# Performance work log

Hardware: AMD Instinct MI355X
Metric: run time of the kernel (lower is better)

The kernel has to match this reference:

```python
import jax, jax.numpy as jnp
import numpy as np

NUM_HEADS = 8
WIN = (7, 7)


def _relative_position_index(wh, ww):
    # Same construction as the torch module (numpy, static).
    coords = np.stack(np.meshgrid(np.arange(wh), np.arange(ww), indexing='ij'))  # (2, wh, ww)
    flat = coords.reshape(2, -1)                                                 # (2, L)
    rel = flat[:, :, None] - flat[:, None, :]                                    # (2, L, L)
    rel = rel.transpose(1, 2, 0).astype(np.int64)                                # (L, L, 2)
    rel[:, :, 0] += wh - 1
    rel[:, :, 1] += ww - 1
    rel[:, :, 0] *= 2 * ww - 1
    return rel.sum(-1)  # (L, L), values in [0, (2wh-1)*(2ww-1))


def setup_inputs() -> dict:
    key = jax.random.key(0)
    k0, k1, k2, k3, k4 = jax.random.split(key, 5)
    B, C = 2048, 256
    wh, ww = WIN
    L = wh * ww
    nW = 64
    q = jax.random.normal(k0, (B, C, wh, ww), dtype=jnp.float32)
    k = jax.random.normal(k1, (B, C, wh, ww), dtype=jnp.float32)
    v = jax.random.normal(k2, (B, C, wh, ww), dtype=jnp.float32)
    # Swin-style shift mask: 0 where attend, -100 where blocked
    keep = jax.random.uniform(k3, (nW, L, L)) < 0.9
    mask = jnp.where(keep, 0.0, -100.0).astype(jnp.float32)
    n_bias = (2 * wh - 1) * (2 * ww - 1)  # 169
    rel_bias_table = 0.02 * jax.random.normal(k4, (n_bias, NUM_HEADS), dtype=jnp.float32)
    rel_pos_index = jnp.asarray(_relative_position_index(wh, ww), dtype=jnp.int32)
    return {"q": q, "k": k, "v": v, "mask": mask,
            "rel_bias_table": rel_bias_table, "rel_pos_index": rel_pos_index}


def reference(q, k, v, mask, rel_bias_table, rel_pos_index):
    b, c, wh, ww = q.shape
    L = wh * ww
    H = NUM_HEADS
    d_k = c // H
    scale = d_k ** -0.5
    qh = q.reshape(b, H, d_k, L)
    kh = k.reshape(b, H, d_k, L)
    # NOTE: the original torch code reassigns v = k.reshape(...) — values come from k.
    vh = kh
    attn = jnp.einsum('bhct,bhcs->bhts', qh, kh) * scale  # (b, H, L, L)
    bias = rel_bias_table[rel_pos_index.reshape(-1)].reshape(L, L, H)
    attn = attn + jnp.transpose(bias, (2, 0, 1))[None]    # (1, H, L, L)
    nW = mask.shape[0]
    attn = attn.reshape(b // nW, nW, H, L, L) + mask[None, :, None]
    attn = attn.reshape(b, H, L, L)
    attn = jax.nn.softmax(attn, axis=-1)
    score = jnp.einsum('bhts,bhcs->bhct', attn, vh).reshape(b, c, wh, ww)
    return (score, attn)
```

## Files before the change

### kernel.cpp

```cpp
#include <hip/hip_runtime.h>
#include <hip/hip_bf16.h>
#include <math.h>


#define LW 49
#define NH 8

typedef short s16x8 __attribute__((ext_vector_type(8)));
typedef float f32x4 __attribute__((ext_vector_type(4)));
typedef unsigned short u16x4 __attribute__((ext_vector_type(4)));

union Frag { s16x8 v; unsigned short u[8]; };

__device__ __forceinline__ unsigned short f2bf(float x) {
    return __builtin_bit_cast(unsigned short, __float2bfloat16(x));
}
__device__ __forceinline__ float bf2f(unsigned short h) {
    return __uint_as_float(((unsigned)h) << 16);
}
__device__ __forceinline__ void split8(const float* xf, Frag& hi, Frag& lo) {
    #pragma unroll
    for (int j = 0; j < 8; j++) {
        const unsigned short hb = f2bf(xf[j]);
        hi.u[j] = hb;
        lo.u[j] = f2bf(xf[j] - bf2f(hb));
    }
}

__device__ __forceinline__ void lds_barrier() {
    asm volatile("s_waitcnt lgkmcnt(0)" ::: "memory");
    __builtin_amdgcn_s_barrier();
    asm volatile("" ::: "memory");
    __builtin_amdgcn_sched_barrier(0);
}
__device__ __forceinline__ void stage_barrier() {
    asm volatile("s_waitcnt vmcnt(0) lgkmcnt(0)" ::: "memory");
    __builtin_amdgcn_s_barrier();
    asm volatile("" ::: "memory");
    __builtin_amdgcn_sched_barrier(0);
}

__device__ __forceinline__ void load_lds16(const void* g, void* l) {
    __builtin_amdgcn_global_load_lds(
        (const __attribute__((address_space(1))) void*)g,
        (__attribute__((address_space(3))) void*)l, 16, 0, 0);
}

#define MFMA16(A, B, C) __builtin_amdgcn_mfma_f32_16x16x32_bf16((A), (B), (C), 0, 0, 0)

__global__ __launch_bounds__(256) void prep_frag_kernel(
    const float* __restrict__ mask, const float* __restrict__ table,
    const int* __restrict__ idx,
    unsigned short* __restrict__ biasB, unsigned short* __restrict__ maskB)
{
    const int i = blockIdx.x * 256 + threadIdx.x;
    const int NBF = 8 * 4096;
    const int NMF = 64 * 4096;
    const float L2E = 1.4426950408889634f;
    if (i < NBF) {
        const int h = i >> 12, rem = i & 4095;
        const int gi = rem >> 8, lane = (rem >> 2) & 63, r = rem & 3;
        const int mt = gi >> 2, nt = gi & 3;
        const int t = mt * 16 + (lane >> 4) * 4 + r;
        const int s = nt * 16 + (lane & 15);
        const float v = (t < LW && s < LW)
                      ? table[idx[t * LW + s] * NH + h] * L2E : 0.f;
        biasB[i] = f2bf(v);
    } else if (i < NBF + NMF) {
        const int j = i - NBF;
        const int w2 = j >> 12, rem = j & 4095;
        const int gi = rem >> 8, lane = (rem >> 2) & 63, r = rem & 3;
        const int mt = gi >> 2, nt = gi & 3;
        const int t = mt * 16 + (lane >> 4) * 4 + r;
        const int s = nt * 16 + (lane & 15);
        const float v = (t < LW && s < LW)
                      ? mask[w2 * (LW * LW) + t * LW + s] * L2E : 0.f;
        maskB[j] = f2bf(v);
    }
}

__global__ __launch_bounds__(128, 4) void wa_mfma_kernel(
    const float* __restrict__ q, const float* __restrict__ k,
    const unsigned short* __restrict__ biasB,
    const unsigned short* __restrict__ maskB,
    float* __restrict__ score_out, float* __restrict__ attn_out)
{
    __shared__ __align__(16) char sRaw[12800];

    const int wv   = __builtin_amdgcn_readfirstlane((int)(threadIdx.x >> 6));
    const int bh   = blockIdx.x;
    const int h    = bh & 7;
    const int w    = (bh >> 3) & 63;
    const int tid  = (int)threadIdx.x;
    const int lane = tid & 63;
    const int l15  = lane & 15;
    const int g4   = lane >> 4;

    const float* qp = q + (size_t)bh * (32 * LW);
    const float* kp = k + (size_t)bh * (32 * LW);

    char* ldsK = sRaw;
    char* ldsQ = sRaw + 6400;

    {
        const char* src = (wv == 0) ? (const char*)kp : (const char*)qp;
        char*       dst = (wv == 0) ? ldsK : ldsQ;
        #pragma unroll
        for (int i = 0; i < 6; i++)
            load_lds16(src + i * 1024 + lane * 16, dst + i * 1024);
        if (lane < 16) {
            const int off = (lane < 8) ? lane * 16 : 112;
            load_lds16(src + 6144 + off, dst + 6144);
        }
    }

    stage_barrier();

    u16x4 bq4[2][4], mq4[2][4];
    {
        const unsigned short* bF = biasB + (size_t)h * 4096 + lane * 4;
        const unsigned short* mF = maskB + (size_t)w * 4096 + lane * 4;
        #pragma unroll
        for (int mi = 0; mi < 2; mi++)
            #pragma unroll
            for (int nt = 0; nt < 4; nt++) {
                const int gi = (wv * 2 + mi) * 4 + nt;
                bq4[mi][nt] = *(const u16x4*)(bF + gi * 256);
                mq4[mi][nt] = *(const u16x4*)(mF + gi * 256);
            }
    }

    const float* sKf = (const float*)ldsK;
    const float* sQf = (const float*)ldsQ;

    Frag Qh[2], Ql[2];
    #pragma unroll
    for (int mi = 0; mi < 2; mi++) {
        const int t  = (wv * 2 + mi) * 16 + l15;
        const int tc = t < LW ? t : (LW - 1);
        float xf[8];
        #pragma unroll
        for (int j = 0; j < 8; j++) xf[j] = sQf[(g4 * 8 + j) * LW + tc];
        split8(xf, Qh[mi], Ql[mi]);
    }

    f32x4 acc[2][4];
    #pragma unroll
    for (int mi = 0; mi < 2; mi++)
        #pragma unroll
        for (int nt = 0; nt < 4; nt++)
            #pragma unroll
            for (int r = 0; r < 4; r++) acc[mi][nt][r] = 0.f;

    #pragma unroll
    for (int nt = 0; nt < 4; nt++) {
        const int s  = nt * 16 + l15;
        const int sc = s < LW ? s : (LW - 1);
        float xf[8];
        #pragma unroll
        for (int j = 0; j < 8; j++) xf[j] = sKf[(g4 * 8 + j) * LW + sc];
        Frag Kh, Kl;
        split8(xf, Kh, Kl);
        #pragma unroll
        for (int mi = 0; mi < 2; mi++) {
            acc[mi][nt] = MFMA16(Qh[mi].v, Kh.v, acc[mi][nt]);
            acc[mi][nt] = MFMA16(Ql[mi].v, Kh.v, acc[mi][nt]);
            acc[mi][nt] = MFMA16(Qh[mi].v, Kl.v, acc[mi][nt]);
        }
    }

    Frag K2h[2], K2l[2];
    {
        const int c = wv * 16 + l15;
        #pragma unroll
        for (int ks = 0; ks < 2; ks++) {
            float xf[8];
            #pragma unroll
            for (int j = 0; j < 8; j++) {
                const int s  = ks * 32 + g4 * 8 + j;
                const int sc = s < LW ? s : (LW - 1);
                xf[j] = sKf[c * LW + sc];
            }
            split8(xf, K2h[ks], K2l[ks]);
        }
    }

    const float scale2 = 0.17677669529663687f * 1.4426950408889634f;
    #pragma unroll
    for (int mi = 0; mi < 2; mi++) {
        #pragma unroll
        for (int nt = 0; nt < 4; nt++) {
            const bool pad = (nt * 16 + l15) >= LW;
            #pragma unroll
            for (int r = 0; r < 4; r++) {
                const float bm = bf2f(bq4[mi][nt][r]) + bf2f(mq4[mi][nt][r]);
                const float v2 = fmaf(acc[mi][nt][r], scale2, bm);
                acc[mi][nt][r] = pad ? -1e30f : v2;
            }
        }
    }

    #pragma unroll
    for (int mi = 0; mi < 2; mi++) {
        #pragma unroll
        for (int r = 0; r < 4; r++) {
            float sm = 0.f;
            #pragma unroll
            for (int nt = 0; nt < 4; nt++) {
                const float p = __builtin_exp2f(acc[mi][nt][r]);
                acc[mi][nt][r] = p;
                sm += p;
            }
            sm += __shfl_xor(sm, 1);
            sm += __shfl_xor(sm, 2);
            sm += __shfl_xor(sm, 4);
            sm += __shfl_xor(sm, 8);
            const float inv = 1.0f / sm;
            #pragma unroll
            for (int nt = 0; nt < 4; nt++) acc[mi][nt][r] *= inv;
        }
    }

    lds_barrier();

    unsigned short* sB = (unsigned short*)sRaw;
    #pragma unroll
    for (int mi = 0; mi < 2; mi++) {
        #pragma unroll
        for (int r = 0; r < 4; r++) {
            const int t = (wv * 2 + mi) * 16 + g4 * 4 + r;
            if (t < LW) {
                #pragma unroll
                for (int nt = 0; nt < 4; nt++) {
                    const int s = nt * 16 + l15;
                    const float p = acc[mi][nt][r];
                    const unsigned short ph = f2bf(p);
                    const unsigned short pl = f2bf(p - bf2f(ph));
                    const unsigned idx = (unsigned)t * 64u
                        + ((((unsigned)s >> 3) ^ ((unsigned)t & 7u)) << 3)
                        + ((unsigned)s & 7u);
                    sB[idx]        = ph;
                    sB[3136 + idx] = pl;
                }
            }
        }
    }

    lds_barrier();

    float* attn_base = attn_out + (size_t)bh * (LW * LW);
    #pragma unroll
    for (int it = 0; it < 19; it++) {
        const int i = it * 128 + tid;
        if (i < LW * LW) {
            const int t = i / LW;
            const int s = i - t * LW;
            const unsigned idx = (unsigned)t * 64u
                + ((((unsigned)s >> 3) ^ ((unsigned)t & 7u)) << 3)
                + ((unsigned)s & 7u);
            attn_base[i] = bf2f(sB[idx]) + bf2f(sB[3136 + idx]);
        }
    }

    f32x4 acc2[4];
    #pragma unroll
    for (int nt = 0; nt < 4; nt++)
        #pragma unroll
        for (int r = 0; r < 4; r++) acc2[nt][r] = 0.f;

    #pragma unroll
    for (int ntt = 0; ntt < 4; ntt++) {
        const int t  = ntt * 16 + l15;
        const int tr = t < LW ? t : (LW - 1);
        #pragma unroll
        for (int ks = 0; ks < 2; ks++) {
            const unsigned base = (unsigned)tr * 64u
                + (((unsigned)(ks * 4 + g4) ^ ((unsigned)tr & 7u)) << 3);
            Frag Ph, Pl;
            Ph.v = *(const s16x8*)&sB[base];
            Pl.v = *(const s16x8*)&sB[3136 + base];
            acc2[ntt] = MFMA16(K2h[ks].v, Ph.v, acc2[ntt]);
            acc2[ntt] = MFMA16(K2l[ks].v, Ph.v, acc2[ntt]);
            acc2[ntt] = MFMA16(K2h[ks].v, Pl.v, acc2[ntt]);
        }
    }

    lds_barrier();

    float* scf = (float*)sRaw;
    #pragma unroll
    for (int ntt = 0; ntt < 4; ntt++) {
        const int t = ntt * 16 + l15;
        if (t < LW) {
            #pragma unroll
            for (int r = 0; r < 4; r++) {
                const int c = wv * 16 + g4 * 4 + r;
                scf[c * LW + t] = acc2[ntt][r];
            }
        }
    }

    lds_barrier();

    {
        float4* dst4 = (float4*)(score_out + (size_t)bh * (32 * LW));
        const float4* src4 = (const float4*)sRaw;
        #pragma unroll
        for (int k2 = 0; k2 < 4; k2++) {
            const int j = k2 * 128 + tid;
            if (j < 392) dst4[j] = src4[j];
        }
    }
}

__global__ __launch_bounds__(256, 4) void wa_fallback_kernel(
    const float* __restrict__ q, const float* __restrict__ k,
    const float* __restrict__ mask0, const float* __restrict__ table,
    const int* __restrict__ idx,
    float* __restrict__ score_out, float* __restrict__ attn_out)
{
    __shared__ float sPf[LW * LW];
    const int lane = threadIdx.x & 63;
    const int wv   = __builtin_amdgcn_readfirstlane((int)(threadIdx.x >> 6));
    const int bh   = blockIdx.x * 4 + wv;
    const int h    = bh & 7;
    const int w    = (bh >> 3) & 63;
    const int t    = lane;
    const int tc   = (t < LW) ? t : (LW - 1);

    const float* qp = q + (size_t)bh * (32 * LW);
    const float* kp = k + (size_t)bh * (32 * LW);

    float qreg[32];
    #pragma unroll
    for (int c = 0; c < 32; c++) qreg[c] = qp[c * LW + tc];

    float S[LW];
    #pragma unroll
    for (int s = 0; s < LW; s++) S[s] = 0.f;
    #pragma unroll
    for (int c = 0; c < 32; c++) {
        #pragma unroll
        for (int s = 0; s < LW; s++)
            S[s] = fmaf(qreg[c], kp[c * LW + s], S[s]);
    }

    const float scale = 0.17677669529663687f;
    const float* mrow = mask0 + (size_t)w * (LW * LW) + tc * LW;
    const int*   irow = idx + tc * LW;
    #pragma unroll
    for (int s = 0; s < LW; s++) {
        const float bm = table[irow[s] * NH + h] + mrow[s];
        S[s] = fmaf(S[s], scale, bm);
    }

    float m = S[0];
    #pragma unroll
    for (int s = 1; s < LW; s++) m = fmaxf(m, S[s]);
    float sum = 0.f;
    #pragma unroll
    for (int s = 0; s < LW; s++) { S[s] = __expf(S[s] - m); sum += S[s]; }
    const float invs = 1.0f / sum;
    #pragma unroll
    for (int s = 0; s < LW; s++) S[s] *= invs;

    float* attn_base = attn_out + (size_t)bh * (LW * LW);
    for (int turn = 0; turn < 4; turn++) {
        __syncthreads();
        if (turn == wv) {
            if (t < LW) {
                #pragma unroll
                for (int s = 0; s < LW; s++) sPf[t * LW + s] = S[s];
            }
            #pragma unroll
            for (int it = 0; it < 38; it++) {
                const int i = it * 64 + lane;
                if (i < LW * LW) attn_base[i] = sPf[i];
            }
        }
    }

    float* sc = score_out + (size_t)bh * (32 * LW);
    #pragma unroll
    for (int c = 0; c < 32; c++) {
        float a = 0.f;
        #pragma unroll
        for (int s = 0; s < LW; s++) a = fmaf(S[s], kp[c * LW + s], a);
        if (t < LW) sc[c * LW + t] = a;
    }
}

extern "C" void kernel_launch(void* const* d_in, const int* in_sizes, int n_in,
                              void* d_out, int out_size, void* d_ws, size_t ws_size,
                              hipStream_t stream) {
    const float* q     = (const float*)d_in[0];
    const float* k     = (const float*)d_in[1];
    const float* mask  = (const float*)d_in[3];
    const float* table = (const float*)d_in[4];
    const int*   idx   = (const int*)d_in[5];

    float* score_out = (float*)d_out;
    float* attn_out  = score_out + (size_t)2048 * 256 * 49;

    const size_t NBF = (size_t)8 * 4096;
    const size_t NMF = (size_t)64 * 4096;

    if (ws_size >= (NBF + NMF) * sizeof(unsigned short)) {
        unsigned short* biasB = (unsigned short*)d_ws;
        unsigned short* maskB = biasB + NBF;
        const int tot = (int)(NBF + NMF);
        prep_frag_kernel<<<(tot + 255) / 256, 256, 0, stream>>>(
            mask, table, idx, biasB, maskB);
        wa_mfma_kernel<<<16384, 128, 0, stream>>>(
            q, k, biasB, maskB, score_out, attn_out);
    } else {
        wa_fallback_kernel<<<4096, 256, 0, stream>>>(
            q, k, mask, table, idx, score_out, attn_out);
    }
}
```

Baseline: 443.7 us.

## Process two heads per block and vectorize bias/mask fragment and output stores

```diff
diff --git a/kernel.cpp b/kernel.cpp
--- a/kernel.cpp
+++ b/kernel.cpp
@@ -8,7 +8,7 @@
 
 typedef short s16x8 __attribute__((ext_vector_type(8)));
 typedef float f32x4 __attribute__((ext_vector_type(4)));
-typedef unsigned short u16x4 __attribute__((ext_vector_type(4)));
+typedef unsigned short u16x8 __attribute__((ext_vector_type(8)));
 
 union Frag { s16x8 v; unsigned short u[8]; };
 
@@ -59,8 +59,8 @@
     const float L2E = 1.4426950408889634f;
     if (i < NBF) {
         const int h = i >> 12, rem = i & 4095;
-        const int gi = rem >> 8, lane = (rem >> 2) & 63, r = rem & 3;
-        const int mt = gi >> 2, nt = gi & 3;
+        const int mt = rem >> 10, lane = (rem >> 4) & 63, e = rem & 15;
+        const int nt = e >> 2, r = e & 3;
         const int t = mt * 16 + (lane >> 4) * 4 + r;
         const int s = nt * 16 + (lane & 15);
         const float v = (t < LW && s < LW)
@@ -69,8 +69,8 @@
     } else if (i < NBF + NMF) {
         const int j = i - NBF;
         const int w2 = j >> 12, rem = j & 4095;
-        const int gi = rem >> 8, lane = (rem >> 2) & 63, r = rem & 3;
-        const int mt = gi >> 2, nt = gi & 3;
+        const int mt = rem >> 10, lane = (rem >> 4) & 63, e = rem & 15;
+        const int nt = e >> 2, r = e & 3;
         const int t = mt * 16 + (lane >> 4) * 4 + r;
         const int s = nt * 16 + (lane & 15);
         const float v = (t < LW && s < LW)
@@ -79,19 +79,21 @@
     }
 }
 
-__global__ __launch_bounds__(128, 4) void wa_mfma_kernel(
+__global__ __launch_bounds__(256, 4) void wa_mfma_kernel(
     const float* __restrict__ q, const float* __restrict__ k,
     const unsigned short* __restrict__ biasB,
     const unsigned short* __restrict__ maskB,
     float* __restrict__ score_out, float* __restrict__ attn_out)
 {
-    __shared__ __align__(16) char sRaw[12800];
-
-    const int wv   = __builtin_amdgcn_readfirstlane((int)(threadIdx.x >> 6));
-    const int bh   = blockIdx.x;
+    __shared__ __align__(16) char sRaw[2][12800];
+
+    const int tid  = (int)threadIdx.x;
+    const int wv   = __builtin_amdgcn_readfirstlane(tid >> 6);
+    const int sub  = wv >> 1;
+    const int wvL  = wv & 1;
+    const int bh   = blockIdx.x * 2 + sub;
     const int h    = bh & 7;
     const int w    = (bh >> 3) & 63;
-    const int tid  = (int)threadIdx.x;
     const int lane = tid & 63;
     const int l15  = lane & 15;
     const int g4   = lane >> 4;
@@ -99,12 +101,13 @@
     const float* qp = q + (size_t)bh * (32 * LW);
     const float* kp = k + (size_t)bh * (32 * LW);
 
-    char* ldsK = sRaw;
-    char* ldsQ = sRaw + 6400;
+    char* ldsBase = &sRaw[sub][0];
+    char* ldsK = ldsBase;
+    char* ldsQ = ldsBase + 6400;
 
     {
-        const char* src = (wv == 0) ? (const char*)kp : (const char*)qp;
-        char*       dst = (wv == 0) ? ldsK : ldsQ;
+        const char* src = (wvL == 0) ? (const char*)kp : (const char*)qp;
+        char*       dst = (wvL == 0) ? ldsK : ldsQ;
         #pragma unroll
         for (int i = 0; i < 6; i++)
             load_lds16(src + i * 1024 + lane * 16, dst + i * 1024);
@@ -116,18 +119,20 @@
 
     stage_barrier();
 
-    u16x4 bq4[2][4], mq4[2][4];
+    u16x8 bq8[2][2], mq8[2][2];
     {
-        const unsigned short* bF = biasB + (size_t)h * 4096 + lane * 4;
-        const unsigned short* mF = maskB + (size_t)w * 4096 + lane * 4;
-        #pragma unroll
-        for (int mi = 0; mi < 2; mi++)
-            #pragma unroll
-            for (int nt = 0; nt < 4; nt++) {
-                const int gi = (wv * 2 + mi) * 4 + nt;
-                bq4[mi][nt] = *(const u16x4*)(bF + gi * 256);
-                mq4[mi][nt] = *(const u16x4*)(mF + gi * 256);
-            }
+        const unsigned short* bF = biasB + (size_t)h * 4096;
+        const unsigned short* mF = maskB + (size_t)w * 4096;
+        #pragma unroll
+        for (int mi = 0; mi < 2; mi++) {
+            const int mt = wvL * 2 + mi;
+            const u16x8* bp = (const u16x8*)(bF + mt * 1024 + lane * 16);
+            const u16x8* mp = (const u16x8*)(mF + mt * 1024 + lane * 16);
+            bq8[mi][0] = bp[0];
+            bq8[mi][1] = bp[1];
+            mq8[mi][0] = mp[0];
+            mq8[mi][1] = mp[1];
+        }
     }
 
     const float* sKf = (const float*)ldsK;
@@ -136,7 +141,7 @@
     Frag Qh[2], Ql[2];
     #pragma unroll
     for (int mi = 0; mi < 2; mi++) {
-        const int t  = (wv * 2 + mi) * 16 + l15;
+        const int t  = (wvL * 2 + mi) * 16 + l15;
         const int tc = t < LW ? t : (LW - 1);
         float xf[8];
         #pragma unroll
@@ -171,7 +176,7 @@
 
     Frag K2h[2], K2l[2];
     {
-        const int c = wv * 16 + l15;
+        const int c = wvL * 16 + l15;
         #pragma unroll
         for (int ks = 0; ks < 2; ks++) {
             float xf[8];
@@ -193,7 +198,8 @@
             const bool pad = (nt * 16 + l15) >= LW;
             #pragma unroll
             for (int r = 0; r < 4; r++) {
-                const float bm = bf2f(bq4[mi][nt][r]) + bf2f(mq4[mi][nt][r]);
+                const float bm = bf2f(bq8[mi][nt >> 1][(nt & 1) * 4 + r])
+                               + bf2f(mq8[mi][nt >> 1][(nt & 1) * 4 + r]);
                 const float v2 = fmaf(acc[mi][nt][r], scale2, bm);
                 acc[mi][nt][r] = pad ? -1e30f : v2;
             }
@@ -223,12 +229,12 @@
 
     lds_barrier();
 
-    unsigned short* sB = (unsigned short*)sRaw;
+    unsigned short* sB = (unsigned short*)ldsBase;
     #pragma unroll
     for (int mi = 0; mi < 2; mi++) {
         #pragma unroll
         for (int r = 0; r < 4; r++) {
-            const int t = (wv * 2 + mi) * 16 + g4 * 4 + r;
+            const int t = (wvL * 2 + mi) * 16 + g4 * 4 + r;
             if (t < LW) {
                 #pragma unroll
                 for (int nt = 0; nt < 4; nt++) {
@@ -248,17 +254,28 @@
 
     lds_barrier();
 
-    float* attn_base = attn_out + (size_t)bh * (LW * LW);
-    #pragma unroll
-    for (int it = 0; it < 19; it++) {
-        const int i = it * 128 + tid;
-        if (i < LW * LW) {
-            const int t = i / LW;
-            const int s = i - t * LW;
-            const unsigned idx = (unsigned)t * 64u
-                + ((((unsigned)s >> 3) ^ ((unsigned)t & 7u)) << 3)
-                + ((unsigned)s & 7u);
-            attn_base[i] = bf2f(sB[idx]) + bf2f(sB[3136 + idx]);
+    {
+        float2* dst2 = (float2*)(attn_out + (size_t)(blockIdx.x * 2) * (LW * LW));
+        #pragma unroll
+        for (int it = 0; it < 10; it++) {
+            const int j = it * 256 + tid;
+            if (j < LW * LW) {
+                float v2[2];
+                #pragma unroll
+                for (int e = 0; e < 2; e++) {
+                    const int g  = 2 * j + e;
+                    const int sg = g >= LW * LW;
+                    const int i2 = g - sg * (LW * LW);
+                    const int t  = i2 / LW;
+                    const int s  = i2 - t * LW;
+                    const unsigned idx = (unsigned)t * 64u
+                        + ((((unsigned)s >> 3) ^ ((unsigned)t & 7u)) << 3)
+                        + ((unsigned)s & 7u);
+                    const unsigned short* sBg = (const unsigned short*)&sRaw[sg][0];
+                    v2[e] = bf2f(sBg[idx]) + bf2f(sBg[3136 + idx]);
+                }
+                dst2[j] = make_float2(v2[0], v2[1]);
+            }
         }
     }
 
@@ -287,14 +304,14 @@
 
     lds_barrier();
 
-    float* scf = (float*)sRaw;
+    float* scf = (float*)ldsBase;
     #pragma unroll
     for (int ntt = 0; ntt < 4; ntt++) {
         const int t = ntt * 16 + l15;
         if (t < LW) {
             #pragma unroll
             for (int r = 0; r < 4; r++) {
-                const int c = wv * 16 + g4 * 4 + r;
+                const int c = wvL * 16 + g4 * 4 + r;
                 scf[c * LW + t] = acc2[ntt][r];
             }
         }
@@ -303,12 +320,15 @@
     lds_barrier();
 
     {
-        float4* dst4 = (float4*)(score_out + (size_t)bh * (32 * LW));
-        const float4* src4 = (const float4*)sRaw;
-        #pragma unroll
-        for (int k2 = 0; k2 < 4; k2++) {
-            const int j = k2 * 128 + tid;
-            if (j < 392) dst4[j] = src4[j];
+        float4* dst4 = (float4*)(score_out + (size_t)(blockIdx.x * 2) * (32 * LW));
+        #pragma unroll
+        for (int it = 0; it < 4; it++) {
+            const int j = it * 256 + tid;
+            if (j < 784) {
+                const int sg = j >= 392;
+                const float4* src4 = (const float4*)&sRaw[sg][0];
+                dst4[j] = src4[j - sg * 392];
+            }
         }
     }
 }
@@ -411,7 +431,7 @@
         const int tot = (int)(NBF + NMF);
         prep_frag_kernel<<<(tot + 255) / 256, 256, 0, stream>>>(
             mask, table, idx, biasB, maskB);
-        wa_mfma_kernel<<<16384, 128, 0, stream>>>(
+        wa_mfma_kernel<<<8192, 256, 0, stream>>>(
             q, k, biasB, maskB, score_out, attn_out);
     } else {
         wa_fallback_kernel<<<4096, 256, 0, stream>>>(
```

Measured after the change: 443.3 us, median of 2. No clear change (-0.1%).
